# Optimization experiments

Measured on AMD Instinct MI355X. Metric: run time of the kernel, lower is better.

## Reference

```python
import jax, jax.numpy as jnp
import numpy as np
import math

C_CURV = 1.0          # manifold curvature c
KH = KW = 3
STRIDE = (1, 1)
PADDING = (1, 1)
DILATION = (1, 1)
IN_CH = 64            # includes time channel
OUT_CH = 64           # excludes time channel


def setup_inputs() -> dict:
    key = jax.random.key(0)
    k1, k2, k3 = jax.random.split(key, 3)
    B, H, W = 32, 64, 64
    x = jax.random.normal(k1, (B, H, W, IN_CH), dtype=jnp.float32)
    kk = KH * KW
    lin_in = (IN_CH - 1) * kk + 1  # 568
    stdv = math.sqrt(2.0 / ((IN_CH - 1) * kk))
    weight = jax.random.uniform(k2, (OUT_CH, lin_in), minval=-stdv, maxval=stdv, dtype=jnp.float32)
    bias = jax.random.uniform(k3, (OUT_CH,), minval=-stdv, maxval=stdv, dtype=jnp.float32)
    return {"x": x, "weight": weight, "bias": bias}


def _im2col(x):
    """x: [B,H,W,C] -> gathered patches [B,h_out,w_out,KH,KW,C] (torch Unfold semantics)."""
    B, H, W, C = x.shape
    xp = jnp.pad(x, ((0, 0), (PADDING[0], PADDING[0]), (PADDING[1], PADDING[1]), (0, 0)))
    h_out = (H + 2 * PADDING[0] - DILATION[0] * (KH - 1) - 1) // STRIDE[0] + 1
    w_out = (W + 2 * PADDING[1] - DILATION[1] * (KW - 1) - 1) // STRIDE[1] + 1
    rows = STRIDE[0] * jnp.arange(h_out)[:, None] + DILATION[0] * jnp.arange(KH)[None, :]  # [h_out,KH]
    cols = STRIDE[1] * jnp.arange(w_out)[:, None] + DILATION[1] * jnp.arange(KW)[None, :]  # [w_out,KW]
    g = xp[:, rows[:, None, :, None], cols[None, :, None, :], :]  # [B,h_out,w_out,KH,KW,C]
    return g, h_out, w_out


def reference(x, weight, bias):
    B = x.shape[0]
    kk = KH * KW
    g, h_out, w_out = _im2col(x)
    L = h_out * w_out
    # Time channel (channel 0) over kernel positions, clamped to sqrt(c)
    t = jnp.maximum(g[..., 0].reshape(B, L, kk), jnp.sqrt(jnp.float32(C_CURV)))
    t_rescaled = jnp.sqrt(jnp.sum(t * t, axis=-1, keepdims=True) - (kk - 1) * C_CURV)
    # Space channels in kernel-major, channel-minor order (matches torch reshape/transpose)
    s = g[..., 1:].reshape(B, L, kk * (IN_CH - 1))
    feat = jnp.concatenate([t_rescaled, s], axis=-1)  # [B, L, 568]
    # LorentzLinear: linear on features, recompute time from space norm
    y_space = jnp.einsum('blf,of->blo', feat, weight) + bias
    y_time = jnp.sqrt(jnp.sum(y_space * y_space, axis=-1, keepdims=True) + C_CURV)
    out = jnp.concatenate([y_time, y_space], axis=-1)
    return out.reshape(B, h_out, w_out, OUT_CH + 1)
```

## Files before the change

### kernel.cpp

```cpp
#include <hip/hip_runtime.h>
#include <cstdint>
#include <cstddef>

typedef __attribute__((ext_vector_type(8))) short short8v;
typedef __attribute__((ext_vector_type(4))) unsigned uint4v;
typedef __attribute__((ext_vector_type(4))) float floatx4;

#define LIN 568

__device__ __forceinline__ short f32_to_bf16(float f) {
  unsigned u = __builtin_bit_cast(unsigned, f);
  u += 0x7fffu + ((u >> 16) & 1u);
  return (short)(u >> 16);
}
__device__ __forceinline__ float bf16_to_f32(short s) {
  return __builtin_bit_cast(float, ((unsigned)(unsigned short)s) << 16);
}
__device__ __forceinline__ unsigned cvt_pk_bf16(float lo, float hi) {
  unsigned r;
  asm("v_cvt_pk_bf16_f32 %0, %1, %2" : "=v"(r) : "v"(lo), "v"(hi));
  return r;
}
template<int CTRL>
__device__ __forceinline__ float dpp_add(float v) {
  int y = __builtin_amdgcn_update_dpp(0, __builtin_bit_cast(int, v), CTRL, 0xF, 0xF, true);
  return v + __builtin_bit_cast(float, y);
}

__global__ void prep_weight(const float* __restrict__ w, short* __restrict__ wfragg) {
  int i = blockIdx.x * 256 + threadIdx.x;
  if (i >= 9 * 2 * 4 * 64 * 8) return;
  int j    = i & 7;
  int lane = (i >> 3) & 63;
  int nb   = (i >> 9) & 3;
  int half = (i >> 11) & 1;
  int tap  = i >> 12;
  int n = nb * 16 + (lane & 15);
  int c = half * 32 + ((lane >> 4) << 3) + j;
  float v = (c == 0) ? 0.0f : w[n * LIN + 1 + tap * 63 + (c - 1)];
  wfragg[i] = f32_to_bf16(v);
}

__launch_bounds__(256, 2)
__global__ void lconv_main(const float* __restrict__ x, const float* __restrict__ w,
                           const float* __restrict__ bias, const short* __restrict__ wfragg,
                           float* __restrict__ out) {
  __shared__ short xt[6 * 66 * 72];
  __shared__ float tres_s[4 * 64];

  const int tid = threadIdx.x;
  const int bb = blockIdx.x >> 4;
  const int h0 = (blockIdx.x & 15) << 2;
  const float* xb = x + (size_t)bb * (64 * 64 * 64);

  const int lane = tid & 63;
  const int l15 = lane & 15;
  const int q = lane >> 4;
  const int wv = tid >> 6;

  float4 s0[12], s1[12];
#pragma unroll
  for (int i = 0; i < 12; ++i) {
    int idx = i * 256 + tid;
    int row = idx >> 9;
    int rem = idx & 511;
    int col = rem >> 3;
    int ch8 = (rem & 7) << 3;
    int h = h0 - 1 + row;
    s0[i] = {0.f, 0.f, 0.f, 0.f};
    s1[i] = {0.f, 0.f, 0.f, 0.f};
    if ((unsigned)h < 64u) {
      const float* p = xb + ((h * 64 + col) * 64 + ch8);
      s0[i] = *(const float4*)p;
      s1[i] = *(const float4*)(p + 4);
    }
  }

  const short* wfl = wfragg + lane * 8;
  short8v b0[4], b1[4], b2[4];
#pragma unroll
  for (int nb = 0; nb < 4; ++nb) {
    b0[nb] = *(const short8v*)(wfl + 0 * 2048 + nb * 512);
    b1[nb] = *(const short8v*)(wfl + 1 * 2048 + nb * 512);
    b2[nb] = *(const short8v*)(wfl + 2 * 2048 + nb * 512);
  }
  float bj[4], w0j[4];
#pragma unroll
  for (int nb = 0; nb < 4; ++nb) {
    int n = nb * 16 + l15;
    bj[nb] = bias[n];
    w0j[nb] = w[n * LIN];
  }

#pragma unroll
  for (int i = 0; i < 8; ++i) {
    int idx = i * 256 + tid;
    int row = idx >> 9;
    int rem = idx & 511;
    int col = rem >> 3;
    int ch8 = (rem & 7) << 3;
    uint4v o;
    o[0] = cvt_pk_bf16(s0[i].x, s0[i].y);
    o[1] = cvt_pk_bf16(s0[i].z, s0[i].w);
    o[2] = cvt_pk_bf16(s1[i].x, s1[i].y);
    o[3] = cvt_pk_bf16(s1[i].z, s1[i].w);
    *(uint4v*)&xt[(row * 66 + col + 1) * 72 + ch8] = o;
  }
  if (tid < 64) {
    int r = tid >> 4;
    int cc = (tid >> 3) & 1;
    int ch8 = (tid & 7) << 3;
    short8v z = {0, 0, 0, 0, 0, 0, 0, 0};
    *(short8v*)&xt[(r * 66 + cc * 65) * 72 + ch8] = z;
  }
  __syncthreads();

  floatx4 acc[4][4];
#pragma unroll
  for (int mb = 0; mb < 4; ++mb)
#pragma unroll
    for (int nb = 0; nb < 4; ++nb) acc[mb][nb] = floatx4{0.f, 0.f, 0.f, 0.f};

  auto do_step = [&](int step) {
    const int tap = step >> 1, half = step & 1;
    const int kh = tap / 3, kw = tap % 3;

    short8v bn[4];
    if (step + 3 < 18) {
#pragma unroll
      for (int nb = 0; nb < 4; ++nb)
        bn[nb] = *(const short8v*)(wfl + (step + 3) * 2048 + nb * 512);
    }

    const short* ab = &xt[((wv + kh) * 66 + kw + l15) * 72 + half * 32 + q * 8];
    short8v a[4];
#pragma unroll
    for (int mb = 0; mb < 4; ++mb)
      a[mb] = *(const short8v*)(ab + mb * 16 * 72);

#pragma unroll
    for (int mb = 0; mb < 4; ++mb) {
#pragma unroll
      for (int nb = 0; nb < 4; ++nb)
        acc[mb][nb] = __builtin_amdgcn_mfma_f32_16x16x32_bf16(a[mb], b0[nb], acc[mb][nb], 0, 0, 0);
    }
#pragma unroll
    for (int nb = 0; nb < 4; ++nb) { b0[nb] = b1[nb]; b1[nb] = b2[nb]; b2[nb] = bn[nb]; }
  };

#pragma unroll
  for (int step = 0; step < 6; ++step) do_step(step);

#pragma unroll
  for (int i = 8; i < 12; ++i) {
    int idx = i * 256 + tid;
    int row = idx >> 9;
    int rem = idx & 511;
    int col = rem >> 3;
    int ch8 = (rem & 7) << 3;
    uint4v o;
    o[0] = cvt_pk_bf16(s0[i].x, s0[i].y);
    o[1] = cvt_pk_bf16(s0[i].z, s0[i].w);
    o[2] = cvt_pk_bf16(s1[i].x, s1[i].y);
    o[3] = cvt_pk_bf16(s1[i].z, s1[i].w);
    *(uint4v*)&xt[(row * 66 + col + 1) * 72 + ch8] = o;
  }
  if (tid < 32) {
    int r = 4 + (tid >> 4);
    int cc = (tid >> 3) & 1;
    int ch8 = (tid & 7) << 3;
    short8v z = {0, 0, 0, 0, 0, 0, 0, 0};
    *(short8v*)&xt[(r * 66 + cc * 65) * 72 + ch8] = z;
  }
  __syncthreads();

#pragma unroll
  for (int step = 6; step < 18; ++step) do_step(step);

  {
    float ss = 0.f;
#pragma unroll
    for (int dh = 0; dh < 3; ++dh)
#pragma unroll
      for (int dw = 0; dw < 3; ++dw) {
        float tv = bf16_to_f32(xt[((wv + dh) * 66 + lane + dw) * 72]);
        tv = fmaxf(tv, 1.0f);
        ss += tv * tv;
      }
    tres_s[wv * 64 + lane] = sqrtf(ss - 8.0f);
  }

#pragma unroll
  for (int mb = 0; mb < 4; ++mb) {
    float4 t4 = *(const float4*)&tres_s[wv * 64 + mb * 16 + q * 4];
#pragma unroll
    for (int r = 0; r < 4; ++r) {
      int pcol = mb * 16 + q * 4 + r;
      float tr = t4[r];
      float v0 = acc[mb][0][r] + bj[0] + tr * w0j[0];
      float v1 = acc[mb][1][r] + bj[1] + tr * w0j[1];
      float v2 = acc[mb][2][r] + bj[2] + tr * w0j[2];
      float v3 = acc[mb][3][r] + bj[3] + tr * w0j[3];
      float ss = v0 * v0 + v1 * v1 + v2 * v2 + v3 * v3;
      ss = dpp_add<0xB1>(ss);
      ss = dpp_add<0x4E>(ss);
      ss = dpp_add<0x141>(ss);
      ss = dpp_add<0x140>(ss);
      float* ob = out + (size_t)((bb * 64 + h0 + wv) * 64 + pcol) * 65;
      if (l15 == 0) ob[0] = sqrtf(ss + 1.0f);
      ob[1 + l15]  = v0;
      ob[17 + l15] = v1;
      ob[33 + l15] = v2;
      ob[49 + l15] = v3;
    }
  }
}

extern "C" void kernel_launch(void* const* d_in, const int* in_sizes, int n_in,
                              void* d_out, int out_size, void* d_ws, size_t ws_size,
                              hipStream_t stream) {
  const float* x = (const float*)d_in[0];
  const float* w = (const float*)d_in[1];
  const float* b = (const float*)d_in[2];
  float* out = (float*)d_out;
  short* wfragg = (short*)d_ws;

  prep_weight<<<144, 256, 0, stream>>>(w, wfragg);
  lconv_main<<<32 * 16, 256, 0, stream>>>(x, w, b, wfragg, out);
}
```

Measured before the change: 96.47 us.

## Load conv input directly from global into MFMA fragments, dropping LDS staging

```diff
diff --git a/kernel.cpp b/kernel.cpp
--- a/kernel.cpp
+++ b/kernel.cpp
@@ -12,9 +12,6 @@
   unsigned u = __builtin_bit_cast(unsigned, f);
   u += 0x7fffu + ((u >> 16) & 1u);
   return (short)(u >> 16);
-}
-__device__ __forceinline__ float bf16_to_f32(short s) {
-  return __builtin_bit_cast(float, ((unsigned)(unsigned short)s) << 16);
 }
 __device__ __forceinline__ unsigned cvt_pk_bf16(float lo, float hi) {
   unsigned r;
@@ -45,7 +42,6 @@
 __global__ void lconv_main(const float* __restrict__ x, const float* __restrict__ w,
                            const float* __restrict__ bias, const short* __restrict__ wfragg,
                            float* __restrict__ out) {
-  __shared__ short xt[6 * 66 * 72];
   __shared__ float tres_s[4 * 64];
 
   const int tid = threadIdx.x;
@@ -58,24 +54,6 @@
   const int q = lane >> 4;
   const int wv = tid >> 6;
 
-  float4 s0[12], s1[12];
-#pragma unroll
-  for (int i = 0; i < 12; ++i) {
-    int idx = i * 256 + tid;
-    int row = idx >> 9;
-    int rem = idx & 511;
-    int col = rem >> 3;
-    int ch8 = (rem & 7) << 3;
-    int h = h0 - 1 + row;
-    s0[i] = {0.f, 0.f, 0.f, 0.f};
-    s1[i] = {0.f, 0.f, 0.f, 0.f};
-    if ((unsigned)h < 64u) {
-      const float* p = xb + ((h * 64 + col) * 64 + ch8);
-      s0[i] = *(const float4*)p;
-      s1[i] = *(const float4*)(p + 4);
-    }
-  }
-
   const short* wfl = wfragg + lane * 8;
   short8v b0[4], b1[4], b2[4];
 #pragma unroll
@@ -92,38 +70,46 @@
     w0j[nb] = w[n * LIN];
   }
 
-#pragma unroll
-  for (int i = 0; i < 8; ++i) {
-    int idx = i * 256 + tid;
-    int row = idx >> 9;
-    int rem = idx & 511;
-    int col = rem >> 3;
-    int ch8 = (rem & 7) << 3;
-    uint4v o;
-    o[0] = cvt_pk_bf16(s0[i].x, s0[i].y);
-    o[1] = cvt_pk_bf16(s0[i].z, s0[i].w);
-    o[2] = cvt_pk_bf16(s1[i].x, s1[i].y);
-    o[3] = cvt_pk_bf16(s1[i].z, s1[i].w);
-    *(uint4v*)&xt[(row * 66 + col + 1) * 72 + ch8] = o;
-  }
-  if (tid < 64) {
-    int r = tid >> 4;
-    int cc = (tid >> 3) & 1;
-    int ch8 = (tid & 7) << 3;
-    short8v z = {0, 0, 0, 0, 0, 0, 0, 0};
-    *(short8v*)&xt[(r * 66 + cc * 65) * 72 + ch8] = z;
-  }
-  __syncthreads();
-
   floatx4 acc[4][4];
 #pragma unroll
   for (int mb = 0; mb < 4; ++mb)
 #pragma unroll
     for (int nb = 0; nb < 4; ++nb) acc[mb][nb] = floatx4{0.f, 0.f, 0.f, 0.f};
 
-  auto do_step = [&](int step) {
+  float4 av0[2][4], av1[2][4];
+
+  auto issue_A = [&](int step) {
+    if (step >= 18) return;
+    const int par = step & 1;
     const int tap = step >> 1, half = step & 1;
     const int kh = tap / 3, kw = tap % 3;
+    const int h = h0 + wv + kh - 1;
+    if ((unsigned)h < 64u) {
+      const float* rp = xb + (h * 64) * 64 + half * 32 + q * 8;
+#pragma unroll
+      for (int mb = 0; mb < 4; ++mb) {
+        int col = mb * 16 + l15 + kw - 1;
+        int cc = col < 0 ? 0 : (col > 63 ? 63 : col);
+        const float* p = rp + cc * 64;
+        av0[par][mb] = *(const float4*)p;
+        av1[par][mb] = *(const float4*)(p + 4);
+      }
+    } else {
+#pragma unroll
+      for (int mb = 0; mb < 4; ++mb) {
+        av0[par][mb] = {0.f, 0.f, 0.f, 0.f};
+        av1[par][mb] = {0.f, 0.f, 0.f, 0.f};
+      }
+    }
+  };
+
+  issue_A(0);
+
+#pragma unroll
+  for (int step = 0; step < 18; ++step) {
+    const int par = step & 1;
+    const int tap = step >> 1;
+    const int kw = tap % 3;
 
     short8v bn[4];
     if (step + 3 < 18) {
@@ -132,11 +118,21 @@
         bn[nb] = *(const short8v*)(wfl + (step + 3) * 2048 + nb * 512);
     }
 
-    const short* ab = &xt[((wv + kh) * 66 + kw + l15) * 72 + half * 32 + q * 8];
     short8v a[4];
 #pragma unroll
-    for (int mb = 0; mb < 4; ++mb)
-      a[mb] = *(const short8v*)(ab + mb * 16 * 72);
+    for (int mb = 0; mb < 4; ++mb) {
+      uint4v o;
+      o[0] = cvt_pk_bf16(av0[par][mb].x, av0[par][mb].y);
+      o[1] = cvt_pk_bf16(av0[par][mb].z, av0[par][mb].w);
+      o[2] = cvt_pk_bf16(av1[par][mb].x, av1[par][mb].y);
+      o[3] = cvt_pk_bf16(av1[par][mb].z, av1[par][mb].w);
+      a[mb] = __builtin_bit_cast(short8v, o);
+    }
+    short8v z = {0, 0, 0, 0, 0, 0, 0, 0};
+    if (kw == 0 && l15 == 0)  a[0] = z;
+    if (kw == 2 && l15 == 15) a[3] = z;
+
+    issue_A(step + 1);
 
 #pragma unroll
     for (int mb = 0; mb < 4; ++mb) {
@@ -146,47 +142,27 @@
     }
 #pragma unroll
     for (int nb = 0; nb < 4; ++nb) { b0[nb] = b1[nb]; b1[nb] = b2[nb]; b2[nb] = bn[nb]; }
-  };
-
-#pragma unroll
-  for (int step = 0; step < 6; ++step) do_step(step);
-
-#pragma unroll
-  for (int i = 8; i < 12; ++i) {
-    int idx = i * 256 + tid;
-    int row = idx >> 9;
-    int rem = idx & 511;
-    int col = rem >> 3;
-    int ch8 = (rem & 7) << 3;
-    uint4v o;
-    o[0] = cvt_pk_bf16(s0[i].x, s0[i].y);
-    o[1] = cvt_pk_bf16(s0[i].z, s0[i].w);
-    o[2] = cvt_pk_bf16(s1[i].x, s1[i].y);
-    o[3] = cvt_pk_bf16(s1[i].z, s1[i].w);
-    *(uint4v*)&xt[(row * 66 + col + 1) * 72 + ch8] = o;
-  }
-  if (tid < 32) {
-    int r = 4 + (tid >> 4);
-    int cc = (tid >> 3) & 1;
-    int ch8 = (tid & 7) << 3;
-    short8v z = {0, 0, 0, 0, 0, 0, 0, 0};
-    *(short8v*)&xt[(r * 66 + cc * 65) * 72 + ch8] = z;
-  }
-  __syncthreads();
-
-#pragma unroll
-  for (int step = 6; step < 18; ++step) do_step(step);
+  }
 
   {
     float ss = 0.f;
 #pragma unroll
-    for (int dh = 0; dh < 3; ++dh)
-#pragma unroll
-      for (int dw = 0; dw < 3; ++dw) {
-        float tv = bf16_to_f32(xt[((wv + dh) * 66 + lane + dw) * 72]);
-        tv = fmaxf(tv, 1.0f);
-        ss += tv * tv;
+    for (int dh = 0; dh < 3; ++dh) {
+      int hh = h0 + wv + dh - 1;
+      if ((unsigned)hh < 64u) {
+#pragma unroll
+        for (int dw = 0; dw < 3; ++dw) {
+          int c = lane + dw - 1;
+          int cc = c < 0 ? 0 : (c > 63 ? 63 : c);
+          float tv = xb[(hh * 64 + cc) * 64];
+          tv = ((unsigned)c < 64u) ? tv : 0.f;
+          tv = fmaxf(tv, 1.0f);
+          ss += tv * tv;
+        }
+      } else {
+        ss += 3.0f;
       }
+    }
     tres_s[wv * 64 + lane] = sqrtf(ss - 8.0f);
   }
 
```

Measured after the change: 122.7 us. 1.27x slower.
